# Kernel optimization log

Hardware: AMD Instinct MI355X
Metric: run time of the kernel (lower is better)

Reference implementation:

```python
import jax, jax.numpy as jnp
import numpy as np

EPS = 1e-07
NEG = -1e9


def setup_inputs() -> dict:
    key = jax.random.key(0)
    k1, k2, k3, k4 = jax.random.split(key, 4)
    N, M, D = 8192, 8192, 128
    xi = jax.random.normal(k1, (N, D), dtype=jnp.float32)
    xj = jax.random.normal(k2, (M, D), dtype=jnp.float32)
    adj = jax.random.randint(k3, (N, M), 0, 2, dtype=jnp.int32)
    beta = jax.random.uniform(k4, (1,), dtype=jnp.float32)
    return {"xi": xi, "xj": xj, "adj": adj, "beta": beta}


def reference(xi, xj, adj, beta):
    # cosine similarity scores, scaled by learned beta
    xi_norm = jnp.linalg.norm(xi, ord=2, axis=1, keepdims=True)      # [N,1]
    xj_norm = jnp.linalg.norm(xj, ord=2, axis=1, keepdims=True).T    # [1,M]
    cos = beta * (xi @ xj.T) / (xi_norm * xj_norm + EPS)             # [N,M]
    # additive adjacency mask: non-edges pushed to -1e9
    mask = (1.0 - adj.astype(cos.dtype)) * NEG
    P = jax.nn.softmax(cos + mask, axis=1)                           # [N,M]
    return P @ xj                                                    # [N,D]
```

## Files before the change

### kernel.cpp

```cpp
#include <hip/hip_runtime.h>
#include <hip/hip_bf16.h>

typedef float f32x4 __attribute__((ext_vector_type(4)));
typedef short s16x8 __attribute__((ext_vector_type(8)));
typedef unsigned long long ull;

#define NROWS 8192
#define MCOLS 8192
#define DIM   128
#define JSPLIT 16
#define JCHUNK 512
#define KVB    64
#define ITERS  8

typedef __attribute__((address_space(3))) unsigned int lds_u32;
typedef __attribute__((address_space(1))) unsigned int g_u32;

__device__ __forceinline__ void gl_lds16(const void* g, void* l) {
    __builtin_amdgcn_global_load_lds((const g_u32*)g, (lds_u32*)l, 16, 0, 0);
}

__global__ void prep_scale_both(const float* __restrict__ xi,
                                const float* __restrict__ xj,
                                const float* __restrict__ beta,
                                __hip_bfloat16* __restrict__ Qbf,
                                __hip_bfloat16* __restrict__ Kbf) {
    int gr = blockIdx.x * 4 + (threadIdx.x >> 6);
    int l = threadIdx.x & 63;
    const float* src;
    __hip_bfloat16* dst;
    int row;
    if (gr < NROWS) { row = gr;          src = xi; dst = Qbf; }
    else            { row = gr - NROWS;  src = xj; dst = Kbf; }
    const float* xr = src + (size_t)row * DIM;
    float x0 = xr[l], x1 = xr[l + 64];
    float ss = x0 * x0 + x1 * x1;
#pragma unroll
    for (int off = 32; off >= 1; off >>= 1) ss += __shfl_xor(ss, off);
    float s = 1.0f / sqrtf(ss);
    if (gr < NROWS) s *= beta[0];
    __hip_bfloat16* o = dst + (size_t)row * DIM;
    o[l]      = __float2bfloat16(x0 * s);
    o[l + 64] = __float2bfloat16(x1 * s);
}

__global__ void prep_vt(const float* __restrict__ xj, __hip_bfloat16* __restrict__ vt) {
    __shared__ float tile[64][65];
    int j0 = blockIdx.x * 64;
    int d0 = blockIdx.y * 64;
    int t = threadIdx.x;
#pragma unroll
    for (int c = 0; c < 16; ++c) {
        int idx = t + 256 * c;
        int jr = idx >> 6, dc = idx & 63;
        tile[jr][dc] = xj[(size_t)(j0 + jr) * DIM + d0 + dc];
    }
    __syncthreads();
#pragma unroll
    for (int c = 0; c < 16; ++c) {
        int idx = t + 256 * c;
        int dr = idx >> 6, jc = idx & 63;
        vt[(size_t)(d0 + dr) * MCOLS + j0 + jc] = __float2bfloat16(tile[jc][dr]);
    }
}

__global__ __launch_bounds__(256) void pack_adj8(const int* __restrict__ adj,
                                                 ull* __restrict__ bm) {
    const int lane = threadIdx.x & 63;
    const int gw = (int)((blockIdx.x * 256 + threadIdx.x) >> 6);
#pragma unroll 2
    for (int s = 0; s < 32; ++s) {
        int win = gw + s * 8192;
        const int* base = adj + (size_t)win * 256;
        int a0 = base[lane], a1 = base[64 + lane], a2 = base[128 + lane], a3 = base[192 + lane];
        ull b0 = __ballot(a0 != 0);
        ull b1 = __ballot(a1 != 0);
        ull b2 = __ballot(a2 != 0);
        ull b3 = __ballot(a3 != 0);
        if (lane < 4) {
            ull v = (lane == 0) ? b0 : ((lane == 1) ? b1 : ((lane == 2) ? b2 : b3));
            bm[(size_t)win * 4 + lane] = v;
        }
    }
}

__global__ __launch_bounds__(256, 3) void flash8(const __hip_bfloat16* __restrict__ Qbf,
                                                 const __hip_bfloat16* __restrict__ Kbf,
                                                 const __hip_bfloat16* __restrict__ Vt,
                                                 const ull* __restrict__ bm,
                                                 float* __restrict__ Opart,
                                                 float* __restrict__ Lpart) {
    __shared__ char smem[41984];
    unsigned short* Klds = (unsigned short*)smem;
    unsigned short* Vlds = (unsigned short*)(smem + 16384);
    __hip_bfloat16* Plds = (__hip_bfloat16*)(smem + 32768);

    const int tid  = threadIdx.x;
    const int w    = tid >> 6;
    const int lane = tid & 63;
    const int g    = lane >> 4;
    const int ln   = lane & 15;
    const int bid  = blockIdx.x;
    const int jc   = bid & (JSPLIT - 1);
    const int rt   = bid >> 4;
    const int wrow = rt * 64 + w * 16;
    const int jbase = jc * JCHUNK;

    s16x8 qf[4];
#pragma unroll
    for (int kt = 0; kt < 4; ++kt)
        qf[kt] = *(const s16x8*)(Qbf + (size_t)(wrow + ln) * DIM + kt * 32 + g * 8);

    f32x4 zero = {0.f, 0.f, 0.f, 0.f};
    f32x4 acc[8];
#pragma unroll
    for (int dt = 0; dt < 8; ++dt) acc[dt] = zero;
    float lr[4] = {0.f, 0.f, 0.f, 0.f};

    __hip_bfloat16* pme = Plds + w * (16 * 72);

    for (int it = 0; it < ITERS; ++it) {
        const int jt = jbase + it * KVB;

#pragma unroll
        for (int p = 0; p < 4; ++p) {
            int S = p * 256 + tid;
            int row = S >> 4, u = S & 15;
            const char* src = (const char*)Kbf + (((size_t)(jt + row)) << 8) + ((u ^ (row & 7)) << 4);
            gl_lds16(src, smem + p * 4096 + w * 1024);
        }
#pragma unroll
        for (int p = 0; p < 4; ++p) {
            int S = p * 256 + tid;
            int row = S >> 3, u = S & 7;
            const char* src = (const char*)Vt + (((size_t)row) << 14) + (((size_t)jt) << 1) + ((u ^ (row & 7)) << 4);
            gl_lds16(src, smem + 16384 + p * 4096 + w * 1024);
        }
        __syncthreads();

        ull mw[4];
#pragma unroll
        for (int r = 0; r < 4; ++r)
            mw[r] = bm[(size_t)(wrow + g * 4 + r) * 128 + (jt >> 6)];

        f32x4 s4[4];
#pragma unroll
        for (int ct = 0; ct < 4; ++ct) {
            f32x4 s = zero;
#pragma unroll
            for (int kt = 0; kt < 4; ++kt) {
                int row = ct * 16 + ln;
                s16x8 kf = *(const s16x8*)(Klds + row * 128 + (((kt * 4 + g) ^ (ln & 7)) << 3));
                s = __builtin_amdgcn_mfma_f32_16x16x32_bf16(qf[kt], kf, s, 0, 0, 0);
            }
            s4[ct] = s;
        }

#pragma unroll
        for (int r = 0; r < 4; ++r) {
#pragma unroll
            for (int ct = 0; ct < 4; ++ct) {
                float p = ((mw[r] >> (ct * 16 + ln)) & 1) ? __expf(s4[ct][r]) : 0.f;
                lr[r] += p;
                pme[(g * 4 + r) * 72 + ct * 16 + ln] = __float2bfloat16(p);
            }
        }

#pragma unroll
        for (int kt2 = 0; kt2 < 2; ++kt2) {
            s16x8 pf = *(const s16x8*)(pme + ln * 72 + kt2 * 32 + g * 8);
#pragma unroll
            for (int dt = 0; dt < 8; ++dt) {
                int row = dt * 16 + ln;
                s16x8 vf = *(const s16x8*)(Vlds + row * 64 + (((kt2 * 4 + g) ^ (ln & 7)) << 3));
                acc[dt] = __builtin_amdgcn_mfma_f32_16x16x32_bf16(pf, vf, acc[dt], 0, 0, 0);
            }
        }
        __syncthreads();
    }

#pragma unroll
    for (int r = 0; r < 4; ++r) {
        lr[r] += __shfl_xor(lr[r], 1);
        lr[r] += __shfl_xor(lr[r], 2);
        lr[r] += __shfl_xor(lr[r], 4);
        lr[r] += __shfl_xor(lr[r], 8);
    }

    float* ob = Opart + ((size_t)jc * NROWS + wrow + g * 4) * DIM;
#pragma unroll
    for (int r = 0; r < 4; ++r)
#pragma unroll
        for (int dt = 0; dt < 8; ++dt)
            ob[(size_t)r * DIM + dt * 16 + ln] = acc[dt][r];
    if (ln == 0) {
#pragma unroll
        for (int r = 0; r < 4; ++r)
            Lpart[(size_t)jc * NROWS + wrow + g * 4 + r] = lr[r];
    }
}

__global__ __launch_bounds__(256) void merge8(const float* __restrict__ Opart,
                                              const float* __restrict__ Lpart,
                                              float* __restrict__ out) {
    int gid = blockIdx.x * 256 + threadIdx.x;
    int row = gid >> 5;
    int dq  = (gid & 31) * 4;
    float4 sum = {0.f, 0.f, 0.f, 0.f};
    float L = 0.f;
#pragma unroll
    for (int jc = 0; jc < JSPLIT; ++jc) {
        float4 v = *(const float4*)(Opart + ((size_t)jc * NROWS + row) * DIM + dq);
        sum.x += v.x; sum.y += v.y; sum.z += v.z; sum.w += v.w;
        L += Lpart[(size_t)jc * NROWS + row];
    }
    float inv = 1.0f / fmaxf(L, 1e-37f);
    float4 ov = {sum.x * inv, sum.y * inv, sum.z * inv, sum.w * inv};
    *(float4*)(out + (size_t)row * DIM + dq) = ov;
}

extern "C" void kernel_launch(void* const* d_in, const int* in_sizes, int n_in,
                              void* d_out, int out_size, void* d_ws, size_t ws_size,
                              hipStream_t stream) {
    const float* xi   = (const float*)d_in[0];
    const float* xj   = (const float*)d_in[1];
    const int*   adj  = (const int*)d_in[2];
    const float* beta = (const float*)d_in[3];
    float* out = (float*)d_out;

    char* ws = (char*)d_ws;
    __hip_bfloat16* Qbf = (__hip_bfloat16*)ws;
    __hip_bfloat16* Kbf = (__hip_bfloat16*)(ws + (size_t)NROWS * DIM * 2);
    __hip_bfloat16* Vt  = (__hip_bfloat16*)(ws + 2 * (size_t)NROWS * DIM * 2);
    ull*            bm  = (ull*)(ws + 3 * (size_t)NROWS * DIM * 2);
    float*          Op  = (float*)(ws + 3 * (size_t)NROWS * DIM * 2 + (size_t)NROWS * (MCOLS / 8));
    float*          Lp  = (float*)((char*)Op + (size_t)JSPLIT * NROWS * DIM * 4);

    hipLaunchKernelGGL(pack_adj8, dim3(2048), dim3(256), 0, stream, adj, bm);
    hipLaunchKernelGGL(prep_scale_both, dim3(4096), dim3(256), 0, stream, xi, xj, beta, Qbf, Kbf);
    hipLaunchKernelGGL(prep_vt, dim3(128, 2), dim3(256), 0, stream, xj, Vt);
    hipLaunchKernelGGL(flash8, dim3(128 * JSPLIT), dim3(256), 0, stream, Qbf, Kbf, Vt, bm, Op, Lp);
    hipLaunchKernelGGL(merge8, dim3(1024), dim3(256), 0, stream, Op, Lp, out);
}
```

Before: 137.0 us.

## Fuse prep kernels and double-buffer K/V tiles with halved J split

Merges the three preprocessing kernels (normalize/scale, V transpose, adjacency bit-packing) into one launch to cut launch overhead. The flash kernel now double-buffers K/V tiles in LDS, issuing the next tile's async global-to-LDS loads before computing the current one, so load latency overlaps compute. JSPLIT drops from 16 to 8 with longer chunks, which halves partial-output traffic in the merge. The cost is roughly 73KB of LDS per block, which lowers occupancy (launch bounds go from 3 to 2 blocks per CU), plus a wasted prefetch on the final iteration.

```diff
diff --git a/kernel.cpp b/kernel.cpp
--- a/kernel.cpp
+++ b/kernel.cpp
@@ -8,10 +8,10 @@
 #define NROWS 8192
 #define MCOLS 8192
 #define DIM   128
-#define JSPLIT 16
-#define JCHUNK 512
+#define JSPLIT 8
+#define JCHUNK 1024
 #define KVB    64
-#define ITERS  8
+#define ITERS  16
 
 typedef __attribute__((address_space(3))) unsigned int lds_u32;
 typedef __attribute__((address_space(1))) unsigned int g_u32;
@@ -20,54 +20,62 @@
     __builtin_amdgcn_global_load_lds((const g_u32*)g, (lds_u32*)l, 16, 0, 0);
 }
 
-__global__ void prep_scale_both(const float* __restrict__ xi,
-                                const float* __restrict__ xj,
-                                const float* __restrict__ beta,
-                                __hip_bfloat16* __restrict__ Qbf,
-                                __hip_bfloat16* __restrict__ Kbf) {
-    int gr = blockIdx.x * 4 + (threadIdx.x >> 6);
-    int l = threadIdx.x & 63;
-    const float* src;
-    __hip_bfloat16* dst;
-    int row;
-    if (gr < NROWS) { row = gr;          src = xi; dst = Qbf; }
-    else            { row = gr - NROWS;  src = xj; dst = Kbf; }
-    const float* xr = src + (size_t)row * DIM;
-    float x0 = xr[l], x1 = xr[l + 64];
-    float ss = x0 * x0 + x1 * x1;
-#pragma unroll
-    for (int off = 32; off >= 1; off >>= 1) ss += __shfl_xor(ss, off);
-    float s = 1.0f / sqrtf(ss);
-    if (gr < NROWS) s *= beta[0];
-    __hip_bfloat16* o = dst + (size_t)row * DIM;
-    o[l]      = __float2bfloat16(x0 * s);
-    o[l + 64] = __float2bfloat16(x1 * s);
-}
-
-__global__ void prep_vt(const float* __restrict__ xj, __hip_bfloat16* __restrict__ vt) {
+__global__ __launch_bounds__(256) void prep_all(const float* __restrict__ xi,
+                                                const float* __restrict__ xj,
+                                                const float* __restrict__ beta,
+                                                const int* __restrict__ adj,
+                                                __hip_bfloat16* __restrict__ Qbf,
+                                                __hip_bfloat16* __restrict__ Kbf,
+                                                __hip_bfloat16* __restrict__ Vt,
+                                                ull* __restrict__ bm) {
     __shared__ float tile[64][65];
-    int j0 = blockIdx.x * 64;
-    int d0 = blockIdx.y * 64;
-    int t = threadIdx.x;
-#pragma unroll
-    for (int c = 0; c < 16; ++c) {
-        int idx = t + 256 * c;
-        int jr = idx >> 6, dc = idx & 63;
-        tile[jr][dc] = xj[(size_t)(j0 + jr) * DIM + d0 + dc];
-    }
-    __syncthreads();
-#pragma unroll
-    for (int c = 0; c < 16; ++c) {
-        int idx = t + 256 * c;
-        int dr = idx >> 6, jc = idx & 63;
-        vt[(size_t)(d0 + dr) * MCOLS + j0 + jc] = __float2bfloat16(tile[jc][dr]);
-    }
-}
-
-__global__ __launch_bounds__(256) void pack_adj8(const int* __restrict__ adj,
-                                                 ull* __restrict__ bm) {
-    const int lane = threadIdx.x & 63;
-    const int gw = (int)((blockIdx.x * 256 + threadIdx.x) >> 6);
+    const int tid  = threadIdx.x;
+    const int w    = tid >> 6;
+    const int lane = tid & 63;
+
+    {
+        float b = beta[0];
+#pragma unroll
+        for (int sub = 0; sub < 2; ++sub) {
+            int gr = blockIdx.x * 8 + w * 2 + sub;
+            const float* src;
+            __hip_bfloat16* dst;
+            int row;
+            if (gr < NROWS) { row = gr;          src = xi; dst = Qbf; }
+            else            { row = gr - NROWS;  src = xj; dst = Kbf; }
+            const float* xr = src + (size_t)row * DIM;
+            float x0 = xr[lane], x1 = xr[lane + 64];
+            float ss = x0 * x0 + x1 * x1;
+#pragma unroll
+            for (int off = 32; off >= 1; off >>= 1) ss += __shfl_xor(ss, off);
+            float s = 1.0f / sqrtf(ss);
+            if (gr < NROWS) s *= b;
+            __hip_bfloat16* o = dst + (size_t)row * DIM;
+            o[lane]      = __float2bfloat16(x0 * s);
+            o[lane + 64] = __float2bfloat16(x1 * s);
+        }
+    }
+
+    if (blockIdx.x < 256) {
+        int j0 = (blockIdx.x & 127) * 64;
+        int d0 = (blockIdx.x >> 7) * 64;
+#pragma unroll
+        for (int c = 0; c < 16; ++c) {
+            int idx = tid + 256 * c;
+            int jr = idx >> 6, dc = idx & 63;
+            tile[jr][dc] = xj[(size_t)(j0 + jr) * DIM + d0 + dc];
+        }
+        __syncthreads();
+#pragma unroll
+        for (int c = 0; c < 16; ++c) {
+            int idx = tid + 256 * c;
+            int dr = idx >> 6, jc = idx & 63;
+            Vt[(size_t)(d0 + dr) * MCOLS + j0 + jc] = __float2bfloat16(tile[jc][dr]);
+        }
+        __syncthreads();
+    }
+
+    const int gw = (int)((blockIdx.x * 256 + tid) >> 6);
 #pragma unroll 2
     for (int s = 0; s < 32; ++s) {
         int win = gw + s * 8192;
@@ -84,16 +92,14 @@
     }
 }
 
-__global__ __launch_bounds__(256, 3) void flash8(const __hip_bfloat16* __restrict__ Qbf,
+__global__ __launch_bounds__(256, 2) void flash9(const __hip_bfloat16* __restrict__ Qbf,
                                                  const __hip_bfloat16* __restrict__ Kbf,
                                                  const __hip_bfloat16* __restrict__ Vt,
                                                  const ull* __restrict__ bm,
                                                  float* __restrict__ Opart,
                                                  float* __restrict__ Lpart) {
-    __shared__ char smem[41984];
-    unsigned short* Klds = (unsigned short*)smem;
-    unsigned short* Vlds = (unsigned short*)(smem + 16384);
-    __hip_bfloat16* Plds = (__hip_bfloat16*)(smem + 32768);
+    __shared__ char smem[74752];
+    __hip_bfloat16* Plds = (__hip_bfloat16*)(smem + 65536);
 
     const int tid  = threadIdx.x;
     const int w    = tid >> 6;
@@ -102,7 +108,7 @@
     const int ln   = lane & 15;
     const int bid  = blockIdx.x;
     const int jc   = bid & (JSPLIT - 1);
-    const int rt   = bid >> 4;
+    const int rt   = bid >> 3;
     const int wrow = rt * 64 + w * 16;
     const int jbase = jc * JCHUNK;
 
@@ -119,29 +125,42 @@
 
     __hip_bfloat16* pme = Plds + w * (16 * 72);
 
-    for (int it = 0; it < ITERS; ++it) {
-        const int jt = jbase + it * KVB;
-
+    auto STAGE = [&](int jt, int b) {
+        char* kb = smem + b * 32768;
+        char* vb = kb + 16384;
 #pragma unroll
         for (int p = 0; p < 4; ++p) {
             int S = p * 256 + tid;
             int row = S >> 4, u = S & 15;
-            const char* src = (const char*)Kbf + (((size_t)(jt + row)) << 8) + ((u ^ (row & 7)) << 4);
-            gl_lds16(src, smem + p * 4096 + w * 1024);
+            gl_lds16((const char*)Kbf + (((size_t)(jt + row)) << 8) + ((u ^ (row & 7)) << 4),
+                     kb + p * 4096 + w * 1024);
         }
 #pragma unroll
         for (int p = 0; p < 4; ++p) {
             int S = p * 256 + tid;
             int row = S >> 3, u = S & 7;
-            const char* src = (const char*)Vt + (((size_t)row) << 14) + (((size_t)jt) << 1) + ((u ^ (row & 7)) << 4);
-            gl_lds16(src, smem + 16384 + p * 4096 + w * 1024);
-        }
-        __syncthreads();
+            gl_lds16((const char*)Vt + (((size_t)row) << 14) + (((size_t)jt) << 1) + ((u ^ (row & 7)) << 4),
+                     vb + p * 4096 + w * 1024);
+        }
+    };
+
+    STAGE(jbase, 0);
+    __syncthreads();
+    int cur = 0;
+
+    for (int it = 0; it < ITERS; ++it) {
+        const int jt = jbase + it * KVB;
 
         ull mw[4];
 #pragma unroll
         for (int r = 0; r < 4; ++r)
             mw[r] = bm[(size_t)(wrow + g * 4 + r) * 128 + (jt >> 6)];
+        __builtin_amdgcn_sched_barrier(0);
+
+        STAGE(jbase + ((it + 1) & (ITERS - 1)) * KVB, cur ^ 1);
+
+        unsigned short* Klds = (unsigned short*)(smem + cur * 32768);
+        unsigned short* Vlds = (unsigned short*)(smem + cur * 32768 + 16384);
 
         f32x4 s4[4];
 #pragma unroll
@@ -176,7 +195,9 @@
                 acc[dt] = __builtin_amdgcn_mfma_f32_16x16x32_bf16(pf, vf, acc[dt], 0, 0, 0);
             }
         }
+
         __syncthreads();
+        cur ^= 1;
     }
 
 #pragma unroll
@@ -200,7 +221,7 @@
     }
 }
 
-__global__ __launch_bounds__(256) void merge8(const float* __restrict__ Opart,
+__global__ __launch_bounds__(256) void merge9(const float* __restrict__ Opart,
                                               const float* __restrict__ Lpart,
                                               float* __restrict__ out) {
     int gid = blockIdx.x * 256 + threadIdx.x;
@@ -236,9 +257,7 @@
     float*          Op  = (float*)(ws + 3 * (size_t)NROWS * DIM * 2 + (size_t)NROWS * (MCOLS / 8));
     float*          Lp  = (float*)((char*)Op + (size_t)JSPLIT * NROWS * DIM * 4);
 
-    hipLaunchKernelGGL(pack_adj8, dim3(2048), dim3(256), 0, stream, adj, bm);
-    hipLaunchKernelGGL(prep_scale_both, dim3(4096), dim3(256), 0, stream, xi, xj, beta, Qbf, Kbf);
-    hipLaunchKernelGGL(prep_vt, dim3(128, 2), dim3(256), 0, stream, xj, Vt);
-    hipLaunchKernelGGL(flash8, dim3(128 * JSPLIT), dim3(256), 0, stream, Qbf, Kbf, Vt, bm, Op, Lp);
-    hipLaunchKernelGGL(merge8, dim3(1024), dim3(256), 0, stream, Op, Lp, out);
-}
+    hipLaunchKernelGGL(prep_all, dim3(2048), dim3(256), 0, stream, xi, xj, beta, adj, Qbf, Kbf, Vt, bm);
+    hipLaunchKernelGGL(flash9, dim3(128 * JSPLIT), dim3(256), 0, stream, Qbf, Kbf, Vt, bm, Op, Lp);
+    hipLaunchKernelGGL(merge9, dim3(1024), dim3(256), 0, stream, Op, Lp, out);
+}
```

New measurement: 127.4 us. -7.0%, faster.
